# Kernel optimization log

Measured on AMD Instinct MI355X. Metric: run time of the kernel, lower is better.

The kernel has to match this reference:

```python
import jax, jax.numpy as jnp
import numpy as np

DIM = 768
HID = 3072  # 4 * DIM
EPS = 1e-5


def layer_norm(x, w, b):
    mu = jnp.mean(x, axis=-1, keepdims=True)
    var = jnp.var(x, axis=-1, keepdims=True)
    return (x - mu) * jax.lax.rsqrt(var + EPS) * w + b


def setup_inputs() -> dict:
    key = jax.random.key(0)
    ks = jax.random.split(key, 8)
    C, H = DIM, HID
    s = lambda fan_in: 1.0 / np.sqrt(fan_in)
    return {
        "x": jax.random.normal(ks[0], (32, 577, C), dtype=jnp.float32),
        "norm1_w": jnp.ones((C,), jnp.float32),
        "norm1_b": jnp.zeros((C,), jnp.float32),
        "qkv_w": jax.random.uniform(ks[1], (3 * C, C), jnp.float32, -s(C), s(C)),
        "proj_w": jax.random.uniform(ks[2], (C, C), jnp.float32, -s(C), s(C)),
        "proj_b": jax.random.uniform(ks[3], (C,), jnp.float32, -s(C), s(C)),
        "norm2_w": jnp.ones((C,), jnp.float32),
        "norm2_b": jnp.zeros((C,), jnp.float32),
        "fc1_w": jax.random.uniform(ks[4], (H, C), jnp.float32, -s(C), s(C)),
        "fc1_b": jax.random.uniform(ks[5], (H,), jnp.float32, -s(C), s(C)),
        "fc2_w": jax.random.uniform(ks[6], (C, H), jnp.float32, -s(H), s(H)),
        "fc2_b": jax.random.uniform(ks[7], (C,), jnp.float32, -s(H), s(H)),
    }


def reference(x, norm1_w, norm1_b, qkv_w, proj_w, proj_b,
              norm2_w, norm2_b, fc1_w, fc1_b, fc2_w, fc2_b):
    B, N, C = x.shape
    attn_size = int((N - 1) ** 0.5)
    scale = C ** -0.5

    # --- Attention on norm1(x) (single head) ---
    h = layer_norm(x, norm1_w, norm1_b)
    qkv = (h @ qkv_w.T).reshape(B, N, 3, C)           # [B,N,3,C]
    q, k, v = qkv[:, :, 0], qkv[:, :, 1], qkv[:, :, 2]
    attn = jax.nn.softmax(jnp.einsum('bnc,bmc->bnm', q, k) * scale, axis=-1)
    y = jnp.einsum('bnm,bmc->bnc', attn, v)           # [B,N,C]
    # Faithful to torch: .transpose(1,2).reshape(B,N,C) scrambles layout
    y = jnp.transpose(y, (0, 2, 1)).reshape(B, N, C)
    a = y @ proj_w.T + proj_b
    token_attn = attn[:, 0, 1:].reshape(B, 1, attn_size, attn_size)

    # Faithful to torch Block: input residual is discarded, attention out doubled
    x = a + a

    # --- MLP (exact GELU, as nn.GELU default) ---
    m = layer_norm(x, norm2_w, norm2_b)
    m = jax.nn.gelu(m @ fc1_w.T + fc1_b, approximate=False)
    m = m @ fc2_w.T + fc2_b
    x = x + m
    return (x, token_attn)
```

## Files before the change

### kernel.cpp

```cpp
#include <hip/hip_runtime.h>
#include <hip/hip_bf16.h>

#define Bz   32
#define Nn_  577
#define Np   640
#define Cc   768
#define Hh   3072
#define Mrows (Bz * Nn_)
#define OUT_X (Mrows * Cc)
#define SCALE 0.03608439182435161f

typedef unsigned short ushort_t;
typedef short short8 __attribute__((ext_vector_type(8)));
typedef float f32x4 __attribute__((ext_vector_type(4)));

__device__ __forceinline__ ushort_t f2b(float f) {
    __hip_bfloat16 h = __float2bfloat16(f);
    return *reinterpret_cast<ushort_t*>(&h);
}

__device__ __forceinline__ float gelu_f(float v) {
    float z  = v * 0.70710678118654752f;
    float az = fabsf(z);
    float t_ = __builtin_amdgcn_rcpf(1.f + 0.3275911f * az);
    float y  = t_ * (0.254829592f + t_ * (-0.284496736f + t_ * (1.421413741f +
               t_ * (-1.453152027f + t_ * 1.061405429f))));
    float e  = __expf(-az * az);
    float er = 1.f - y * e;
    er = (z < 0.f) ? -er : er;
    return 0.5f * v * (1.f + er);
}

__device__ __forceinline__ void gl16(const ushort_t* g, ushort_t* l) {
    __builtin_amdgcn_global_load_lds(
        (const __attribute__((address_space(1))) void*)g,
        (__attribute__((address_space(3))) void*)l, 16, 0, 0);
}

__device__ __forceinline__ float bsum(float v, float* sm) {
    #pragma unroll
    for (int o = 32; o > 0; o >>= 1) v += __shfl_down(v, o, 64);
    int lane = threadIdx.x & 63, wid = threadIdx.x >> 6;
    if (lane == 0) sm[wid] = v;
    __syncthreads();
    float r = sm[0] + sm[1] + sm[2] + sm[3];
    __syncthreads();
    return r;
}
__device__ __forceinline__ float bmax(float v, float* sm) {
    #pragma unroll
    for (int o = 32; o > 0; o >>= 1) v = fmaxf(v, __shfl_down(v, o, 64));
    int lane = threadIdx.x & 63, wid = threadIdx.x >> 6;
    if (lane == 0) sm[wid] = v;
    __syncthreads();
    float r = fmaxf(fmaxf(sm[0], sm[1]), fmaxf(sm[2], sm[3]));
    __syncthreads();
    return r;
}

__global__ void cvt_kernel(const float* __restrict__ in, ushort_t* __restrict__ out, int n) {
    int i = blockIdx.x * 256 + threadIdx.x;
    if (i < n) out[i] = f2b(in[i]);
}

__global__ void ln_bf16(const float* __restrict__ x, const float* __restrict__ w,
                        const float* __restrict__ b, ushort_t* __restrict__ out) {
    __shared__ float sm[8];
    long long row = blockIdx.x;
    const float* xr = x + row * Cc;
    float v[3]; float s = 0.f;
    #pragma unroll
    for (int i = 0; i < 3; ++i) { v[i] = xr[threadIdx.x + i * 256]; s += v[i]; }
    float mu = bsum(s, sm) * (1.f / (float)Cc);
    float sq = 0.f;
    #pragma unroll
    for (int i = 0; i < 3; ++i) { float d = v[i] - mu; sq += d * d; }
    float var = bsum(sq, sm + 4) * (1.f / (float)Cc);
    float inv = rsqrtf(var + 1e-5f);
    ushort_t* orow = out + row * Cc;
    #pragma unroll
    for (int i = 0; i < 3; ++i) {
        int c = threadIdx.x + i * 256;
        orow[c] = f2b((v[i] - mu) * inv * w[c] + b[c]);
    }
}

__global__ void softmax_bf16(const float* __restrict__ Sf, ushort_t* __restrict__ Sb,
                             float* __restrict__ tok) {
    __shared__ float sm[8];
    long long row = blockIdx.x;
    int b_l = (int)(row / Nn_), r = (int)(row - (long long)b_l * Nn_);
    const float* src = Sf + row * Np;
    ushort_t* dst = Sb + row * Np;
    float v[3]; float mx = -1e30f;
    #pragma unroll
    for (int i = 0; i < 3; ++i) {
        int c = threadIdx.x + i * 256;
        v[i] = (c < Nn_) ? src[c] : -1e30f;
        mx = fmaxf(mx, v[i]);
    }
    mx = bmax(mx, sm);
    float s = 0.f;
    #pragma unroll
    for (int i = 0; i < 3; ++i) {
        int c = threadIdx.x + i * 256;
        v[i] = (c < Nn_) ? expf(v[i] - mx) : 0.f;
        s += v[i];
    }
    s = bsum(s, sm + 4);
    float inv = 1.f / s;
    #pragma unroll
    for (int i = 0; i < 3; ++i) {
        int c = threadIdx.x + i * 256;
        float p = v[i] * inv;
        if (c < Np) dst[c] = (c < Nn_) ? f2b(p) : (ushort_t)0;
        if (r == 0 && c >= 1 && c < Nn_) tok[(long long)b_l * 576 + (c - 1)] = p;
    }
}

#define EPS_STORE  0
#define EPS_X2     1
#define EPS_GELU   2
#define EPS_ADD    3
#define EPS_QKV    4

#define MM_STAGE(AS, BS, k0) do {            \
    gl16(Ag0 + (k0), &AS[e0]);               \
    gl16(Ag1 + (k0), &AS[e1]);               \
    gl16(Bg0 + (k0), &BS[e0]);               \
    gl16(Bg1 + (k0), &BS[e1]);               \
} while (0)

#define MM_COMPUTE(AS, BS) do {                                             \
    short8 af[4], bfr[4];                                                   \
    _Pragma("unroll")                                                       \
    for (int i = 0; i < 4; ++i) {                                           \
        int r = wr + i * 16 + fr;                                           \
        af[i] = *(const short8*)&AS[r * 32 + ((kq ^ (r & 3)) << 3)];        \
    }                                                                       \
    _Pragma("unroll")                                                       \
    for (int j = 0; j < 4; ++j) {                                           \
        int r = wc + j * 16 + fr;                                           \
        bfr[j] = *(const short8*)&BS[r * 32 + ((kq ^ (r & 3)) << 3)];       \
    }                                                                       \
    _Pragma("unroll")                                                       \
    for (int i = 0; i < 4; ++i)                                             \
        _Pragma("unroll")                                                   \
        for (int j = 0; j < 4; ++j)                                         \
            acc[i][j] = __builtin_amdgcn_mfma_f32_16x16x32_bf16(            \
                af[i], bfr[j], acc[i][j], 0, 0, 0);                         \
} while (0)

template<int EPI, typename OutT>
__global__ __launch_bounds__(256)
void mm_bf16(const ushort_t* __restrict__ A, long long sAb, int lda, int M,
             const ushort_t* __restrict__ B, long long sBb, int ldb, int Nv,
             const float* __restrict__ bias,
             OutT* __restrict__ O, long long sOb, int ldo,
             int K, float alpha,
             ushort_t* __restrict__ qQ, ushort_t* __restrict__ qK, ushort_t* __restrict__ qV)
{
    __shared__ __align__(16) ushort_t As0[128 * 32];
    __shared__ __align__(16) ushort_t As1[128 * 32];
    __shared__ __align__(16) ushort_t Bs0[128 * 32];
    __shared__ __align__(16) ushort_t Bs1[128 * 32];
    const int z = blockIdx.z;
    A += (long long)z * sAb; B += (long long)z * sBb;
    if (O) O += (long long)z * sOb;
    const int n0 = blockIdx.x * 128;
    const int m0 = blockIdx.y * 128;
    const int tid = threadIdx.x;
    const int lane = tid & 63;
    const int wv = tid >> 6;
    const int wr = (wv >> 1) << 6;
    const int wc = (wv & 1) << 6;
    const int fr = lane & 15;
    const int kq = lane >> 4;

    const int e0 = tid * 8, e1 = 2048 + tid * 8;
    const int ra0 = e0 >> 5, qa0 = (((e0 & 31) >> 3) ^ (ra0 & 3)) << 3;
    const int ra1 = e1 >> 5, qa1 = (((e1 & 31) >> 3) ^ (ra1 & 3)) << 3;
    const ushort_t* Ag0 = A + (long long)min(m0 + ra0, M - 1) * lda + qa0;
    const ushort_t* Ag1 = A + (long long)min(m0 + ra1, M - 1) * lda + qa1;
    const ushort_t* Bg0 = B + (long long)min(n0 + ra0, Nv - 1) * ldb + qa0;
    const ushort_t* Bg1 = B + (long long)min(n0 + ra1, Nv - 1) * ldb + qa1;

    f32x4 acc[4][4] = {};
    const int nt = K >> 5;

    MM_STAGE(As0, Bs0, 0);
    __syncthreads();

    for (int t = 0; t < nt; t += 2) {
        MM_STAGE(As1, Bs1, (t + 1) << 5);
        MM_COMPUTE(As0, Bs0);
        __syncthreads();
        if (t + 2 < nt) MM_STAGE(As0, Bs0, (t + 2) << 5);
        MM_COMPUTE(As1, Bs1);
        __syncthreads();
    }

    #pragma unroll
    for (int i = 0; i < 4; ++i) {
        int mb = m0 + wr + i * 16 + (lane >> 4) * 4;
        #pragma unroll
        for (int j = 0; j < 4; ++j) {
            int n = n0 + wc + j * 16 + fr;
            if (n >= Nv) continue;
            f32x4 v4 = acc[i][j];
            #pragma unroll
            for (int r = 0; r < 4; ++r) {
                int m = mb + r;
                if (m >= M) continue;
                float v = v4[r] * alpha;
                if constexpr (EPI == EPS_QKV) {
                    int b_l = m / Nn_, rr = m - b_l * Nn_;
                    if (n < Cc)            qQ[(long long)m * Cc + n] = f2b(v);
                    else if (n < 2 * Cc)   qK[(long long)m * Cc + (n - Cc)] = f2b(v);
                    else                   qV[((long long)b_l * Cc + (n - 2 * Cc)) * Np + rr] = f2b(v);
                } else if constexpr (EPI == EPS_ADD) {
                    if (bias) v += bias[n];
                    long long oi = (long long)m * ldo + n;
                    O[oi] += v;
                } else {
                    if (bias) v += bias[n];
                    if constexpr (EPI == EPS_X2) v *= 2.f;
                    if constexpr (EPI == EPS_GELU) v = gelu_f(v);
                    long long oi = (long long)m * ldo + n;
                    if constexpr (sizeof(OutT) == 2) O[oi] = (OutT)f2b(v);
                    else                             O[oi] = (OutT)v;
                }
            }
        }
    }
}

#define STAGE8(P, h, tt) do {                                        \
    const int ko_ = (tt) * 64 + ((h) >> 1) * 32;                     \
    if (((h) & 1) == 0) {                                            \
        gl16(AsS0 + ko_, &HA[P][(h) >> 1][s0 * 8]);                  \
        gl16(AsS1 + ko_, &HA[P][(h) >> 1][s1 * 8]);                  \
    } else {                                                         \
        gl16(BsS0 + ko_, &HB[P][(h) >> 1][s0 * 8]);                  \
        gl16(BsS1 + ko_, &HB[P][(h) >> 1][s1 * 8]);                  \
    }                                                                \
} while (0)

#define LDA4(P, ks, fbase) do {                                      \
    _Pragma("unroll")                                                \
    for (int f_ = 0; f_ < 4; ++f_)                                   \
        av[f_] = *(const short8*)&HA[P][ks][abase + ((fbase) + f_) * 512]; \
} while (0)

#define LDB4(P, ks) do {                                             \
    _Pragma("unroll")                                                \
    for (int n_ = 0; n_ < 4; ++n_)                                   \
        bv[n_] = *(const short8*)&HB[P][ks][bbase + n_ * 512];       \
} while (0)

#define MFMA16(fbase) do {                                           \
    __builtin_amdgcn_s_setprio(1);                                   \
    _Pragma("unroll")                                                \
    for (int f_ = 0; f_ < 4; ++f_)                                   \
        _Pragma("unroll")                                            \
        for (int n_ = 0; n_ < 4; ++n_)                               \
            acc[(fbase) + f_][n_] = __builtin_amdgcn_mfma_f32_16x16x32_bf16( \
                av[f_], bv[n_], acc[(fbase) + f_][n_], 0, 0, 0);     \
    __builtin_amdgcn_s_setprio(0);                                   \
} while (0)

#define PH_SYNC() do {                                               \
    __builtin_amdgcn_s_barrier();                                    \
    asm volatile("s_waitcnt lgkmcnt(0)" ::: "memory");               \
    __builtin_amdgcn_sched_barrier(0);                               \
} while (0)

template<int EPI, typename OutT>
__global__ __launch_bounds__(512, 1)
void mm256(const ushort_t* __restrict__ A, int lda, int M,
           const ushort_t* __restrict__ B, int ldb, int Nv,
           const float* __restrict__ bias,
           OutT* __restrict__ O, int ldo,
           int K, float alpha,
           ushort_t* __restrict__ qQ, ushort_t* __restrict__ qK, ushort_t* __restrict__ qV)
{
    __shared__ __align__(16) ushort_t HA[2][2][8192];
    __shared__ __align__(16) ushort_t HB[2][2][8192];

    const int nwg = gridDim.x * gridDim.y;
    const int flat = blockIdx.y * gridDim.x + blockIdx.x;
    const int qq = nwg >> 3, rr8 = nwg & 7;
    const int xcd = flat & 7, idx = flat >> 3;
    const int wg = (xcd < rr8 ? xcd * (qq + 1) : rr8 * (qq + 1) + (xcd - rr8) * qq) + idx;
    const int bx = wg % gridDim.x, by = wg / gridDim.x;

    const int n0 = bx * 256, m0 = by * 256;
    const int tid = (int)threadIdx.x;
    const int lane = tid & 63;
    const int wv = tid >> 6;
    const int wm128 = (wv >> 2) * 128;
    const int wn64  = (wv & 3) * 64;
    const int fr = lane & 15;
    const int kq = lane >> 4;

    const int sl    = (kq + 4 * (fr & 1)) ^ (fr >> 1);
    const int lref  = (fr >> 1) * 64 + sl * 8;
    const int abase = wm128 * 32 + lref;
    const int bbase = wn64 * 32 + lref;

    const int s0 = tid, s1 = tid + 512;
    const int line0 = tid >> 3;
    const int u0 = (tid & 7) ^ (line0 & 7);
    const int r0 = (line0 << 1) | (u0 >> 2);
    const int c0 = u0 & 3;
    const ushort_t* AsS0 = A + (long long)min(m0 + r0,       M - 1) * lda + c0 * 8;
    const ushort_t* AsS1 = A + (long long)min(m0 + r0 + 128, M - 1) * lda + c0 * 8;
    const ushort_t* BsS0 = B + (long long)min(n0 + r0,       Nv - 1) * ldb + c0 * 8;
    const ushort_t* BsS1 = B + (long long)min(n0 + r0 + 128, Nv - 1) * ldb + c0 * 8;

    f32x4 acc[8][4] = {};
    const int nt = K >> 6;

    STAGE8(0, 0, 0); STAGE8(0, 1, 0); STAGE8(0, 2, 0); STAGE8(0, 3, 0);
    asm volatile("s_waitcnt vmcnt(4)" ::: "memory");
    __builtin_amdgcn_s_barrier();

    for (int t = 0; t < nt; ++t) {
        const int P = t & 1, Q = P ^ 1;
        const bool pf = (t + 1 < nt);
        short8 av[4], bv[4];

        LDA4(P, 0, 0); LDB4(P, 0);
        if (pf) STAGE8(Q, 0, t + 1);
        PH_SYNC();
        MFMA16(0);
        __builtin_amdgcn_s_barrier();

        LDA4(P, 0, 4);
        if (pf) { STAGE8(Q, 1, t + 1); asm volatile("s_waitcnt vmcnt(4)" ::: "memory"); }
        else    {                      asm volatile("s_waitcnt vmcnt(0)" ::: "memory"); }
        PH_SYNC();
        MFMA16(4);
        __builtin_amdgcn_s_barrier();

        LDA4(P, 1, 0); LDB4(P, 1);
        if (pf) STAGE8(Q, 2, t + 1);
        PH_SYNC();
        MFMA16(0);
        __builtin_amdgcn_s_barrier();

        LDA4(P, 1, 4);
        if (pf) { STAGE8(Q, 3, t + 1); asm volatile("s_waitcnt vmcnt(4)" ::: "memory"); }
        PH_SYNC();
        MFMA16(4);
        __builtin_amdgcn_s_barrier();
    }

    #pragma unroll
    for (int mf = 0; mf < 8; ++mf) {
        int mb = m0 + wm128 + mf * 16 + (lane >> 4) * 4;
        #pragma unroll
        for (int nf = 0; nf < 4; ++nf) {
            int n = n0 + wn64 + nf * 16 + fr;
            if (n >= Nv) continue;
            f32x4 v4 = acc[mf][nf];
            #pragma unroll
            for (int r = 0; r < 4; ++r) {
                int m = mb + r;
                if (m >= M) continue;
                float v = v4[r] * alpha;
                if constexpr (EPI == EPS_QKV) {
                    int b_l = m / Nn_, rq = m - b_l * Nn_;
                    if (n < Cc)            qQ[(long long)m * Cc + n] = f2b(v);
                    else if (n < 2 * Cc)   qK[(long long)m * Cc + (n - Cc)] = f2b(v);
                    else                   qV[((long long)b_l * Cc + (n - 2 * Cc)) * Np + rq] = f2b(v);
                } else if constexpr (EPI == EPS_ADD) {
                    if (bias) v += bias[n];
                    long long oi = (long long)m * ldo + n;
                    O[oi] += v;
                } else {
                    if (bias) v += bias[n];
                    if constexpr (EPI == EPS_X2) v *= 2.f;
                    if constexpr (EPI == EPS_GELU) v = gelu_f(v);
                    long long oi = (long long)m * ldo + n;
                    if constexpr (sizeof(OutT) == 2) O[oi] = (OutT)f2b(v);
                    else                             O[oi] = (OutT)v;
                }
            }
        }
    }
}

extern "C" void kernel_launch(void* const* d_in, const int* in_sizes, int n_in,
                              void* d_out, int out_size, void* d_ws, size_t ws_size,
                              hipStream_t stream) {
    const float* x      = (const float*)d_in[0];
    const float* n1w    = (const float*)d_in[1];
    const float* n1b    = (const float*)d_in[2];
    const float* qkv_w  = (const float*)d_in[3];
    const float* proj_w = (const float*)d_in[4];
    const float* proj_b = (const float*)d_in[5];
    const float* n2w    = (const float*)d_in[6];
    const float* n2b    = (const float*)d_in[7];
    const float* fc1w   = (const float*)d_in[8];
    const float* fc1b   = (const float*)d_in[9];
    const float* fc2w   = (const float*)d_in[10];
    const float* fc2b   = (const float*)d_in[11];
    float* out = (float*)d_out;
    float* x2  = out;
    float* tok = out + OUT_X;

    char* ws = (char*)d_ws;
    const long long nWq = (long long)3 * Cc * Cc;
    const long long nWp = (long long)Cc * Cc;
    const long long nW1 = (long long)Hh * Cc;
    const long long nW2 = (long long)Cc * Hh;
    ushort_t* wq = (ushort_t*)ws;
    ushort_t* wp = wq + nWq;
    ushort_t* w1 = wp + nWp;
    ushort_t* w2 = w1 + nW1;
    const long long WBYTES = 2 * (nWq + nWp + nW1 + nW2);
    char* dyn = ws + WBYTES;
    long long avail = (long long)ws_size - WBYTES;

    const long long perG = 3LL * Nn_ * Cc * 2 + (long long)Cc * Np * 2
                         + (long long)Nn_ * Np * 4 + (long long)Nn_ * Np * 2;
    int G = 1;
    { const int o[6] = {32, 16, 8, 4, 2, 1};
      for (int i = 0; i < 6; ++i) if ((long long)o[i] * perG <= avail) { G = o[i]; break; } }
    int CH = Nn_;
    { const int o[6] = {32, 16, 8, 4, 2, 1};
      for (int i = 0; i < 6; ++i) if ((long long)o[i] * Nn_ * (Cc + Hh) * 2 <= avail) { CH = o[i] * Nn_; break; } }

    ushort_t* hbf = (ushort_t*)dyn;
    ushort_t* Q   = hbf + (long long)G * Nn_ * Cc;
    ushort_t* Kb  = Q   + (long long)G * Nn_ * Cc;
    ushort_t* Vt  = Kb  + (long long)G * Nn_ * Cc;
    float*    Sf  = (float*)(Vt + (long long)G * Cc * Np);
    ushort_t* Sb  = (ushort_t*)(Sf + (long long)G * Nn_ * Np);
    ushort_t* Yt  = hbf;
    ushort_t* g = (ushort_t*)dyn;
    ushort_t* t = g + (long long)CH * Cc;

    cvt_kernel<<<(int)((nWq + 255) / 256), 256, 0, stream>>>(qkv_w, wq, (int)nWq);
    cvt_kernel<<<(int)((nWp + 255) / 256), 256, 0, stream>>>(proj_w, wp, (int)nWp);
    cvt_kernel<<<(int)((nW1 + 255) / 256), 256, 0, stream>>>(fc1w, w1, (int)nW1);
    cvt_kernel<<<(int)((nW2 + 255) / 256), 256, 0, stream>>>(fc2w, w2, (int)nW2);

    for (int b0 = 0; b0 < Bz; b0 += G) {
        const int MR = G * Nn_;
        const int myM256 = (MR + 255) / 256;

        ln_bf16<<<MR, 256, 0, stream>>>(x + (long long)b0 * Nn_ * Cc, n1w, n1b, hbf);

        mm256<EPS_QKV, float><<<dim3(9, myM256, 1), 512, 0, stream>>>(
            hbf, Cc, MR, wq, Cc, 3 * Cc, nullptr,
            (float*)nullptr, Cc, Cc, 1.f, Q, Kb, Vt);

        mm_bf16<EPS_STORE, float><<<dim3(5, 5, G), 256, 0, stream>>>(
            Q, (long long)Nn_ * Cc, Cc, Nn_, Kb, (long long)Nn_ * Cc, Cc, Nn_, nullptr,
            Sf, (long long)Nn_ * Np, Np, Cc, SCALE, nullptr, nullptr, nullptr);

        softmax_bf16<<<MR, 256, 0, stream>>>(Sf, Sb, tok + (long long)b0 * 576);

        mm_bf16<EPS_STORE, ushort_t><<<dim3(5, 6, G), 256, 0, stream>>>(
            Vt, (long long)Cc * Np, Np, Cc, Sb, (long long)Nn_ * Np, Np, Nn_, nullptr,
            Yt, (long long)Cc * Nn_, Nn_, Np, 1.f, nullptr, nullptr, nullptr);

        mm256<EPS_X2, float><<<dim3(3, myM256, 1), 512, 0, stream>>>(
            Yt, Cc, MR, wp, Cc, Cc, proj_b,
            x2 + (long long)b0 * Nn_ * Cc, Cc, Cc, 1.f, nullptr, nullptr, nullptr);
    }

    for (int c0 = 0; c0 < Mrows; c0 += CH) {
        const int cn = (Mrows - c0 < CH) ? (Mrows - c0) : CH;
        const int myC256 = (cn + 255) / 256;

        ln_bf16<<<cn, 256, 0, stream>>>(x2 + (long long)c0 * Cc, n2w, n2b, g);

        mm256<EPS_GELU, ushort_t><<<dim3(12, myC256, 1), 512, 0, stream>>>(
            g, Cc, cn, w1, Cc, Hh, fc1b,
            t, Hh, Cc, 1.f, nullptr, nullptr, nullptr);

        mm256<EPS_ADD, float><<<dim3(3, myC256, 1), 512, 0, stream>>>(
            t, Hh, cn, w2, Hh, Cc, fc2b,
            x2 + (long long)c0 * Cc, Cc, Hh, 1.f, nullptr, nullptr, nullptr);
    }
}
```

Before: 859.6 us.

## Restructure 256x256 GEMM pipeline with A prefetched two tiles ahead and new LDS layout

Rewrites the mm256 main loop so A tiles are staged two k-tiles ahead while B tiles are staged one ahead. Each wave now loads all eight A fragments per k-half into registers. The shared-memory layout changes to 64-element rows with an XOR swizzle, and row-to-buffer mapping is adjusted. Launch bounds are raised to request two workgroups per CU. The aim is to hide global-load latency and cut LDS reads, at the cost of more registers and possible spills under the two-per-CU bound.

```diff
diff --git a/kernel.cpp b/kernel.cpp
--- a/kernel.cpp
+++ b/kernel.cpp
@@ -235,48 +235,47 @@
     }
 }
 
-#define STAGE8(P, h, tt) do {                                        \
-    const int ko_ = (tt) * 64 + ((h) >> 1) * 32;                     \
-    if (((h) & 1) == 0) {                                            \
-        gl16(AsS0 + ko_, &HA[P][(h) >> 1][s0 * 8]);                  \
-        gl16(AsS1 + ko_, &HA[P][(h) >> 1][s1 * 8]);                  \
-    } else {                                                         \
-        gl16(BsS0 + ko_, &HB[P][(h) >> 1][s0 * 8]);                  \
-        gl16(BsS1 + ko_, &HB[P][(h) >> 1][s1 * 8]);                  \
-    }                                                                \
+#define STG_A0(Ts) do { if ((Ts) < nt) { int Pd = (Ts) & 1; int ko = (Ts) * 64; \
+    gl16(gA00 + ko, &HA[Pd][0][tid * 8]);                                       \
+    gl16(gA01 + ko, &HA[Pd][0][tid * 8 + 4096]); } } while (0)
+#define STG_A1(Ts) do { if ((Ts) < nt) { int Pd = (Ts) & 1; int ko = (Ts) * 64; \
+    gl16(gA10 + ko, &HA[Pd][1][tid * 8]);                                       \
+    gl16(gA11 + ko, &HA[Pd][1][tid * 8 + 4096]); } } while (0)
+#define STG_B0(Ts) do { if ((Ts) < nt) { int Pd = (Ts) & 1; int ko = (Ts) * 64; \
+    gl16(gB00 + ko, &HB[Pd][0][tid * 8]);                                       \
+    gl16(gB01 + ko, &HB[Pd][0][tid * 8 + 4096]); } } while (0)
+#define STG_B1(Ts) do { if ((Ts) < nt) { int Pd = (Ts) & 1; int ko = (Ts) * 64; \
+    gl16(gB10 + ko, &HB[Pd][1][tid * 8]);                                       \
+    gl16(gB11 + ko, &HB[Pd][1][tid * 8 + 4096]); } } while (0)
+
+#define RDA8(dst, ckc) do {                                              \
+    _Pragma("unroll")                                                    \
+    for (int mf_ = 0; mf_ < 8; ++mf_)                                    \
+        dst[mf_] = *(const short8*)&HA[P][ha][(mf_ * 16 + fr) * 64 + (ckc)]; \
 } while (0)
-
-#define LDA4(P, ks, fbase) do {                                      \
-    _Pragma("unroll")                                                \
-    for (int f_ = 0; f_ < 4; ++f_)                                   \
-        av[f_] = *(const short8*)&HA[P][ks][abase + ((fbase) + f_) * 512]; \
+#define RDB4(dst, ckc) do {                                              \
+    _Pragma("unroll")                                                    \
+    for (int nf_ = 0; nf_ < 4; ++nf_)                                    \
+        dst[nf_] = *(const short8*)&HB[P][hbh][(nb + nf_ * 16 + fr) * 64 + (ckc)]; \
 } while (0)
 
-#define LDB4(P, ks) do {                                             \
-    _Pragma("unroll")                                                \
-    for (int n_ = 0; n_ < 4; ++n_)                                   \
-        bv[n_] = *(const short8*)&HB[P][ks][bbase + n_ * 512];       \
+#define MM16(mbase, AF, BF) do {                                         \
+    __builtin_amdgcn_s_setprio(1);                                       \
+    _Pragma("unroll")                                                    \
+    for (int i_ = 0; i_ < 4; ++i_)                                       \
+        _Pragma("unroll")                                                \
+        for (int j_ = 0; j_ < 4; ++j_)                                   \
+            acc[(mbase) + i_][j_] = __builtin_amdgcn_mfma_f32_16x16x32_bf16( \
+                AF[(mbase) + i_], BF[j_], acc[(mbase) + i_][j_], 0, 0, 0);   \
+    __builtin_amdgcn_s_setprio(0);                                       \
 } while (0)
 
-#define MFMA16(fbase) do {                                           \
-    __builtin_amdgcn_s_setprio(1);                                   \
-    _Pragma("unroll")                                                \
-    for (int f_ = 0; f_ < 4; ++f_)                                   \
-        _Pragma("unroll")                                            \
-        for (int n_ = 0; n_ < 4; ++n_)                               \
-            acc[(fbase) + f_][n_] = __builtin_amdgcn_mfma_f32_16x16x32_bf16( \
-                av[f_], bv[n_], acc[(fbase) + f_][n_], 0, 0, 0);     \
-    __builtin_amdgcn_s_setprio(0);                                   \
-} while (0)
-
-#define PH_SYNC() do {                                               \
-    __builtin_amdgcn_s_barrier();                                    \
-    asm volatile("s_waitcnt lgkmcnt(0)" ::: "memory");               \
-    __builtin_amdgcn_sched_barrier(0);                               \
-} while (0)
+#define BAR()  __builtin_amdgcn_s_barrier()
+#define LGK0() do { asm volatile("s_waitcnt lgkmcnt(0)" ::: "memory");   \
+                    __builtin_amdgcn_sched_barrier(0); } while (0)
 
 template<int EPI, typename OutT>
-__global__ __launch_bounds__(512, 1)
+__global__ __launch_bounds__(512, 2)
 void mm256(const ushort_t* __restrict__ A, int lda, int M,
            const ushort_t* __restrict__ B, int ldb, int Nv,
            const float* __restrict__ bias,
@@ -298,70 +297,75 @@
     const int tid = (int)threadIdx.x;
     const int lane = tid & 63;
     const int wv = tid >> 6;
-    const int wm128 = (wv >> 2) * 128;
-    const int wn64  = (wv & 3) * 64;
+    const int wm  = (wv >> 2) * 128;
+    const int wn  = (wv & 3) * 64;
+    const int ha  = wv >> 2;
+    const int hbh = (wv & 3) >> 1;
+    const int nb  = wn & 127;
     const int fr = lane & 15;
     const int kq = lane >> 4;
-
-    const int sl    = (kq + 4 * (fr & 1)) ^ (fr >> 1);
-    const int lref  = (fr >> 1) * 64 + sl * 8;
-    const int abase = wm128 * 32 + lref;
-    const int bbase = wn64 * 32 + lref;
-
-    const int s0 = tid, s1 = tid + 512;
-    const int line0 = tid >> 3;
-    const int u0 = (tid & 7) ^ (line0 & 7);
-    const int r0 = (line0 << 1) | (u0 >> 2);
-    const int c0 = u0 & 3;
-    const ushort_t* AsS0 = A + (long long)min(m0 + r0,       M - 1) * lda + c0 * 8;
-    const ushort_t* AsS1 = A + (long long)min(m0 + r0 + 128, M - 1) * lda + c0 * 8;
-    const ushort_t* BsS0 = B + (long long)min(n0 + r0,       Nv - 1) * ldb + c0 * 8;
-    const ushort_t* BsS1 = B + (long long)min(n0 + r0 + 128, Nv - 1) * ldb + c0 * 8;
+    const int fx = fr & 7;
+    const int ck0 = ((0 + kq) ^ fx) * 8;
+    const int ck1 = ((4 + kq) ^ fx) * 8;
+
+    const int r0 = tid >> 3;
+    const int c0 = (tid & 7) ^ (r0 & 7);
+    const ushort_t* gA00 = A + (long long)min(m0 +       r0, M - 1) * lda + c0 * 8;
+    const ushort_t* gA01 = A + (long long)min(m0 +  64 + r0, M - 1) * lda + c0 * 8;
+    const ushort_t* gA10 = A + (long long)min(m0 + 128 + r0, M - 1) * lda + c0 * 8;
+    const ushort_t* gA11 = A + (long long)min(m0 + 192 + r0, M - 1) * lda + c0 * 8;
+    const ushort_t* gB00 = B + (long long)min(n0 +       r0, Nv - 1) * ldb + c0 * 8;
+    const ushort_t* gB01 = B + (long long)min(n0 +  64 + r0, Nv - 1) * ldb + c0 * 8;
+    const ushort_t* gB10 = B + (long long)min(n0 + 128 + r0, Nv - 1) * ldb + c0 * 8;
+    const ushort_t* gB11 = B + (long long)min(n0 + 192 + r0, Nv - 1) * ldb + c0 * 8;
 
     f32x4 acc[8][4] = {};
     const int nt = K >> 6;
 
-    STAGE8(0, 0, 0); STAGE8(0, 1, 0); STAGE8(0, 2, 0); STAGE8(0, 3, 0);
+    STG_A0(0); STG_A1(0); STG_B0(0); STG_B1(0); STG_A0(1); STG_A1(1);
     asm volatile("s_waitcnt vmcnt(4)" ::: "memory");
-    __builtin_amdgcn_s_barrier();
+    __builtin_amdgcn_sched_barrier(0);
+    BAR();
 
     for (int t = 0; t < nt; ++t) {
-        const int P = t & 1, Q = P ^ 1;
-        const bool pf = (t + 1 < nt);
-        short8 av[4], bv[4];
-
-        LDA4(P, 0, 0); LDB4(P, 0);
-        if (pf) STAGE8(Q, 0, t + 1);
-        PH_SYNC();
-        MFMA16(0);
-        __builtin_amdgcn_s_barrier();
-
-        LDA4(P, 0, 4);
-        if (pf) { STAGE8(Q, 1, t + 1); asm volatile("s_waitcnt vmcnt(4)" ::: "memory"); }
-        else    {                      asm volatile("s_waitcnt vmcnt(0)" ::: "memory"); }
-        PH_SYNC();
-        MFMA16(4);
-        __builtin_amdgcn_s_barrier();
-
-        LDA4(P, 1, 0); LDB4(P, 1);
-        if (pf) STAGE8(Q, 2, t + 1);
-        PH_SYNC();
-        MFMA16(0);
-        __builtin_amdgcn_s_barrier();
-
-        LDA4(P, 1, 4);
-        if (pf) { STAGE8(Q, 3, t + 1); asm volatile("s_waitcnt vmcnt(4)" ::: "memory"); }
-        PH_SYNC();
-        MFMA16(4);
-        __builtin_amdgcn_s_barrier();
+        const int P = t & 1;
+        short8 a0[8], a1[8], b0[4], b1[4];
+
+        RDA8(a0, ck0); RDB4(b0, ck0);
+        STG_B0(t + 1);
+        asm volatile("s_waitcnt lgkmcnt(8)" ::: "memory");
+        __builtin_amdgcn_sched_barrier(0);
+        BAR(); LGK0();
+        MM16(0, a0, b0);
+        BAR();
+
+        RDA8(a1, ck1);
+        STG_B1(t + 1);
+        BAR(); LGK0();
+        MM16(4, a0, b0);
+        BAR();
+
+        RDB4(b1, ck1);
+        STG_A0(t + 2);
+        BAR(); LGK0();
+        MM16(0, a1, b1);
+        BAR();
+
+        STG_A1(t + 2);
+        if (t + 2 < nt) { asm volatile("s_waitcnt vmcnt(4)" ::: "memory"); }
+        else            { asm volatile("s_waitcnt vmcnt(0)" ::: "memory"); }
+        __builtin_amdgcn_sched_barrier(0);
+        BAR(); LGK0();
+        MM16(4, a1, b1);
+        BAR();
     }
 
     #pragma unroll
     for (int mf = 0; mf < 8; ++mf) {
-        int mb = m0 + wm128 + mf * 16 + (lane >> 4) * 4;
+        int mb = m0 + wm + mf * 16 + (lane >> 4) * 4;
         #pragma unroll
         for (int nf = 0; nf < 4; ++nf) {
-            int n = n0 + wn64 + nf * 16 + fr;
+            int n = n0 + wn + nf * 16 + fr;
             if (n >= Nv) continue;
             f32x4 v4 = acc[mf][nf];
             #pragma unroll
```

After: 864.2 us. About the same (+0.5%).
